# Kernel optimization log

Measured on AMD Instinct MI355X. Metric: run time of the kernel, lower is better.

Reference implementation:

```python
import jax, jax.numpy as jnp
import numpy as np

D_MODEL = 1024
N_HEADS = 16
HEAD_DIM = D_MODEL // N_HEADS  # 64


def _rotate_half(x):
    x1, x2 = jnp.split(x, 2, axis=-1)
    return jnp.concatenate((-x2, x1), axis=-1)


def setup_inputs() -> dict:
    key = jax.random.key(0)
    ks = jax.random.split(key, 9)
    B, S = 2, 2048
    sc = 1.0 / np.sqrt(D_MODEL)
    return {
        "x": jax.random.normal(ks[0], (B, S, D_MODEL), dtype=jnp.float32),
        "Wq": jax.random.normal(ks[1], (D_MODEL, D_MODEL), dtype=jnp.float32) * sc,
        "bq": jax.random.normal(ks[2], (D_MODEL,), dtype=jnp.float32) * 0.02,
        "Wk": jax.random.normal(ks[3], (D_MODEL, D_MODEL), dtype=jnp.float32) * sc,
        "bk": jax.random.normal(ks[4], (D_MODEL,), dtype=jnp.float32) * 0.02,
        "Wv": jax.random.normal(ks[5], (D_MODEL, D_MODEL), dtype=jnp.float32) * sc,
        "bv": jax.random.normal(ks[6], (D_MODEL,), dtype=jnp.float32) * 0.02,
        "Wo": jax.random.normal(ks[7], (D_MODEL, D_MODEL), dtype=jnp.float32) * sc,
        "bo": jax.random.normal(ks[8], (D_MODEL,), dtype=jnp.float32) * 0.02,
    }


def reference(x, Wq, bq, Wk, bk, Wv, bv, Wo, bo):
    B, S, _ = x.shape
    H, D = N_HEADS, HEAD_DIM
    # QKV projections -> [B, H, S, D]
    q = (x @ Wq + bq).reshape(B, S, H, D).transpose(0, 2, 1, 3)
    k = (x @ Wk + bk).reshape(B, S, H, D).transpose(0, 2, 1, 3)
    v = (x @ Wv + bv).reshape(B, S, H, D).transpose(0, 2, 1, 3)
    # Rotary embedding on head_dim
    inv_freq = 1.0 / (10000.0 ** (jnp.arange(0, D, 2, dtype=jnp.float32) / D))
    t = jnp.arange(S, dtype=jnp.float32)
    freqs = jnp.outer(t, inv_freq)                      # [S, D/2]
    emb = jnp.concatenate((freqs, freqs), axis=-1)      # [S, D]
    # Faithful to torch: cos/sin end up rank-5 [1,1,1,S,D], promoting q/k to [1,B,H,S,D]
    cos = jnp.cos(emb)[None, None, None]
    sin = jnp.sin(emb)[None, None, None]
    qe = q * cos + _rotate_half(q) * sin                # [1,B,H,S,D]
    ke = k * cos + _rotate_half(k) * sin                # [1,B,H,S,D]
    scores = jnp.matmul(qe, jnp.swapaxes(ke, -1, -2)) / np.sqrt(D).astype(np.float32)  # [1,B,H,S,S]
    attn = jax.nn.softmax(scores, axis=-1)
    out = jnp.matmul(attn, v)                           # [1,B,H,S,D] (v broadcast)
    # Faithful replication of torch transpose(1,2).contiguous().view(B,S,d_model)
    out = out.transpose(0, 2, 1, 3, 4).reshape(B, S, H * D)
    return out @ Wo + bo
```

## Files before the change

### kernel.cpp

```cpp
#include <hip/hip_runtime.h>
#include <hip/hip_bf16.h>
#include <stdint.h>

typedef __bf16 bf16;
typedef __bf16 bf16x8 __attribute__((ext_vector_type(8)));
typedef __bf16 bf16x4 __attribute__((ext_vector_type(4)));
typedef float  f32x4  __attribute__((ext_vector_type(4)));
typedef int    i32x4  __attribute__((ext_vector_type(4)));

#define MFMA16(a, b, c) __builtin_amdgcn_mfma_f32_16x16x32_bf16((a), (b), (c), 0, 0, 0)

#define GLOAD16(gp, lp) __builtin_amdgcn_global_load_lds(                     \
    (__attribute__((address_space(1))) void*)(gp),                            \
    (__attribute__((address_space(3))) void*)(lp), 16, 0, 0)


__global__ __launch_bounds__(256) void k_prep(
    const float* __restrict__ x,
    const float* __restrict__ Wq, const float* __restrict__ Wk,
    const float* __restrict__ Wv, const float* __restrict__ Wo,
    bf16* __restrict__ xb, bf16* __restrict__ wqkvt, bf16* __restrict__ wot,
    float* __restrict__ ct, float* __restrict__ st) {
    __shared__ float t[32][33];
    const int bid = blockIdx.x, tid = threadIdx.x;
    if (bid < 4096) {
        const int i = bid * 256 + tid;
        float4 v = ((const float4*)x)[i];
        bf16x4 o;
        o[0] = (bf16)v.x; o[1] = (bf16)v.y; o[2] = (bf16)v.z; o[3] = (bf16)v.w;
        ((bf16x4*)xb)[i] = o;
    } else if (bid < 4352) {
        const int i = (bid - 4096) * 256 + tid;
        const int s = i >> 5, j = i & 31;
        const float inv = expf(-(float)j * (9.210340371976184f / 32.0f));
        const float a = (float)s * inv;
        ct[i] = cosf(a);
        st[i] = sinf(a);
    } else {
        const int wb = bid - 4352;
        const int z = wb >> 10, tb = wb & 1023;
        const float* src = (z == 0) ? Wq : (z == 1) ? Wk : (z == 2) ? Wv : Wo;
        bf16* dst = (z < 3) ? wqkvt + (size_t)z * 1024 * 1024 : wot;
        const int bx = (tb & 31) * 32, by = (tb >> 5) * 32;
        const int tx = tid & 31, ty = tid >> 5;
#pragma unroll
        for (int i = 0; i < 32; i += 8)
            t[ty + i][tx] = src[(size_t)(by + ty + i) * 1024 + bx + tx];
        __syncthreads();
#pragma unroll
        for (int i = 0; i < 32; i += 8)
            dst[(size_t)(bx + ty + i) * 1024 + by + tx] = (bf16)t[tx][ty + i];
    }
}

__device__ __forceinline__ void gemm_loop(const bf16* __restrict__ A,
                                          const bf16* __restrict__ Bt,
                                          int m0, int n0,
                                          bf16* As, bf16* Bs,
                                          f32x4 (&acc)[4][4]) {
    const int tid  = threadIdx.x;
    const int w    = tid >> 6, lane = tid & 63;
    const int wr   = (w >> 1) * 64, wc = (w & 1) * 64;
    const int l15  = lane & 15, l4 = lane >> 4;
    const int srow = w * 16 + (lane >> 2);
    const int skol = 8 * ((lane & 3) ^ ((lane >> 3) & 3));
    const int rdb  = l15 * 32 + 8 * (l4 ^ ((l15 >> 1) & 3));
    const bf16* Ap = A  + (size_t)(m0 + srow) * 1024 + skol;
    const bf16* Bp = Bt + (size_t)(n0 + srow) * 1024 + skol;

#define GSTAGE(B, kt) do {                                                   \
        GLOAD16(Ap + (kt),         As + (B) * 4096 + w * 512);               \
        GLOAD16(Ap + 65536 + (kt), As + (B) * 4096 + 2048 + w * 512);        \
        GLOAD16(Bp + (kt),         Bs + (B) * 4096 + w * 512);               \
        GLOAD16(Bp + 65536 + (kt), Bs + (B) * 4096 + 2048 + w * 512);        \
    } while (0)

#define GTILE(t, B) do {                                                     \
        asm volatile("s_waitcnt vmcnt(0)" ::: "memory");                     \
        __builtin_amdgcn_s_barrier();                                        \
        if ((t) < 31) GSTAGE((B) ^ 1, ((t) + 1) * 32);                       \
        bf16x8 af[4], bfv[4];                                                \
        _Pragma("unroll")                                                    \
        for (int m = 0; m < 4; ++m)                                          \
            af[m] = *(const bf16x8*)(As + (B) * 4096 + (wr + 16 * m) * 32 + rdb); \
        _Pragma("unroll")                                                    \
        for (int n = 0; n < 4; ++n)                                          \
            bfv[n] = *(const bf16x8*)(Bs + (B) * 4096 + (wc + 16 * n) * 32 + rdb); \
        __builtin_amdgcn_s_setprio(1);                                       \
        _Pragma("unroll")                                                    \
        for (int m = 0; m < 4; ++m)                                          \
            _Pragma("unroll")                                                \
            for (int n = 0; n < 4; ++n)                                      \
                acc[m][n] = MFMA16(af[m], bfv[n], acc[m][n]);                \
        __builtin_amdgcn_s_setprio(0);                                       \
    } while (0)

    GSTAGE(0, 0);
    for (int t = 0; t < 32; t += 2) {
        GTILE(t, 0);
        GTILE(t + 1, 1);
    }
#undef GTILE
#undef GSTAGE
}

__global__ __launch_bounds__(256) void k_gemm_qkv(
    const bf16* __restrict__ X, const bf16* __restrict__ Wt,
    const float* __restrict__ bq, const float* __restrict__ bk,
    const float* __restrict__ bv,
    const float* __restrict__ ct, const float* __restrict__ st,
    bf16* __restrict__ qbuf, bf16* __restrict__ kbuf, bf16* __restrict__ vtb) {
    __shared__ __align__(16) bf16 As[2 * 4096];
    __shared__ __align__(16) bf16 Bs[2 * 4096];
    f32x4 acc[4][4] = {};
    const int nwg = gridDim.x * gridDim.y;
    const int wg  = blockIdx.y * gridDim.x + blockIdx.x;
    const int sw  = (wg & 7) * (nwg >> 3) + (wg >> 3);
    const int m0 = (sw / gridDim.x) * 128, n0 = (sw % gridDim.x) * 128;
    gemm_loop(X, Wt, m0, n0, As, Bs, acc);

    const int tid = threadIdx.x;
    const int w = tid >> 6, lane = tid & 63;
    const int wr = (w >> 1) * 64, wc = (w & 1) * 64;
    const int l15 = lane & 15, l4 = lane >> 4;

    const int featbase = n0 + wc;
    const int kind = featbase >> 10;
    const int col0 = featbase & 1023;
    const int h = col0 >> 6;
    const float* bias = (kind == 0) ? bq : (kind == 1) ? bk : bv;
    const float oscale = (kind == 0) ? 0.18033688011112042f : 1.0f;

#pragma unroll
    for (int m = 0; m < 4; ++m) {
#pragma unroll
        for (int j = 0; j < 4; ++j) {
            const int tok = m0 + wr + 16 * m + 4 * l4 + j;
            const int b = tok >> 11, s = tok & 2047;
            float vals[4];
#pragma unroll
            for (int n = 0; n < 4; ++n)
                vals[n] = acc[m][n][j] + bias[col0 + 16 * n + l15];
            if (kind < 2) {
                bf16* dst = (kind == 0) ? qbuf : kbuf;
                const size_t base = ((size_t)((b * 16 + h) * 2048 + s)) * 64;
#pragma unroll
                for (int n = 0; n < 4; ++n) {
                    const int dd = 16 * n + l15;
                    const int jr = dd & 31;
                    const float c = ct[s * 32 + jr], sn = st[s * 32 + jr];
                    const float other = vals[n ^ 2];
                    const float rot = (dd < 32) ? -other : other;
                    dst[base + dd] = (bf16)((vals[n] * c + rot * sn) * oscale);
                }
            } else {
                const int sp = (s & ~63) | ((s & 0x1C) << 1) | ((s & 0x20) >> 3) | (s & 3);
#pragma unroll
                for (int n = 0; n < 4; ++n) {
                    const int dd = 16 * n + l15;
                    vtb[((size_t)((b * 16 + h) * 64 + dd)) * 2048 + sp] = (bf16)vals[n];
                }
            }
        }
    }
}

__global__ __launch_bounds__(512) void k_attn(const bf16* __restrict__ qbuf,
                                              const bf16* __restrict__ kbuf,
                                              const bf16* __restrict__ vtb,
                                              bf16* __restrict__ ob) {
    __shared__ __align__(16) bf16 smem[2 * 2 * 2 * 4096];

    const int tid = threadIdx.x, w = tid >> 6, lane = tid & 63;
    const int team = w >> 2, wt = w & 3;
    const int l15 = lane & 15, l4 = lane >> 4;

    const int sid = blockIdx.x;
    const int bh  = (sid & 7) * 4 + ((sid >> 3) >> 4);
    const int qb0 = ((sid >> 3) & 15) * 128;
    const int b = bh >> 4, h = bh & 15;

    const bf16* qp = qbuf + ((size_t)bh * 2048 + qb0 + wt * 32 + l15) * 64 + 8 * l4;
    i32x4 qr00 = *(const i32x4*)qp;
    i32x4 qr01 = *(const i32x4*)(qp + 32);
    i32x4 qr10 = *(const i32x4*)(qp + 16 * 64);
    i32x4 qr11 = *(const i32x4*)(qp + 16 * 64 + 32);
    asm volatile("" :: "v"(qr00), "v"(qr01), "v"(qr10), "v"(qr11));
    asm volatile("s_waitcnt vmcnt(0)" ::: "memory");
    bf16x8 aq[2][2];
    aq[0][0] = __builtin_bit_cast(bf16x8, qr00);
    aq[0][1] = __builtin_bit_cast(bf16x8, qr01);
    aq[1][0] = __builtin_bit_cast(bf16x8, qr10);
    aq[1][1] = __builtin_bit_cast(bf16x8, qr11);

    bf16x8 ones;
#pragma unroll
    for (int i = 0; i < 8; ++i) ones[i] = (bf16)1.0f;

    f32x4 ao[2][4] = {};
    f32x4 lacc[2] = {};
    const f32x4 zf = {0.f, 0.f, 0.f, 0.f};

    const int r8   = lane >> 3;
    const int skol = 8 * ((lane & 7) ^ r8);
    const int rdb  = l15 * 64 + 32 * ((l15 >> 2) & 1) + 8 * (l4 ^ (l15 & 3));
    const bf16* kp = kbuf + (size_t)bh * 131072 + (size_t)team * 65536
                   + (size_t)(wt * 8 + r8) * 64 + skol;
    const bf16* vp = vtb  + (size_t)bh * 131072 + (size_t)(wt * 8 + r8) * 2048
                   + team * 1024 + skol;
    bf16* sK = smem + team * 16384;
    bf16* sV = smem + team * 16384 + 8192;
    const bf16* pK0 = sK + rdb;
    const bf16* pK1 = sK + (rdb ^ 32);
    const bf16* pV0 = sV + rdb;
    const bf16* pV1 = sV + (rdb ^ 32);

#define STAGE(B, t) do {                                                  \
        GLOAD16(kp + (size_t)(t) * 4096,        sK + (B) * 4096 + wt * 512);        \
        GLOAD16(kp + (size_t)(t) * 4096 + 2048, sK + (B) * 4096 + 2048 + wt * 512); \
        GLOAD16(vp + (t) * 64,                  sV + (B) * 4096 + wt * 512);        \
        GLOAD16(vp + 65536 + (t) * 64,          sV + (B) * 4096 + 2048 + wt * 512); \
    } while (0)

#define TILE(t, B) do {                                                       \
        asm volatile("s_waitcnt vmcnt(0)" ::: "memory");                      \
        __builtin_amdgcn_s_barrier();                                         \
        if ((t) < 15) STAGE((B) ^ 1, (t) + 1);                                \
        bf16x8 kfr[2][4], vfr[2][4];                                          \
        _Pragma("unroll")                                                     \
        for (int n = 0; n < 4; ++n) {                                         \
            kfr[0][n] = *(const bf16x8*)(pK0 + (B) * 4096 + n * 1024);        \
            kfr[1][n] = *(const bf16x8*)(pK1 + (B) * 4096 + n * 1024);        \
            vfr[0][n] = *(const bf16x8*)(pV0 + (B) * 4096 + n * 1024);        \
            vfr[1][n] = *(const bf16x8*)(pV1 + (B) * 4096 + n * 1024);        \
        }                                                                     \
        f32x4 sc[2][4];                                                       \
        __builtin_amdgcn_s_setprio(1);                                        \
        _Pragma("unroll")                                                     \
        for (int n = 0; n < 4; ++n) {                                         \
            sc[0][n] = MFMA16(kfr[0][n], aq[0][0], zf);                       \
            sc[1][n] = MFMA16(kfr[0][n], aq[1][0], zf);                       \
        }                                                                     \
        _Pragma("unroll")                                                     \
        for (int n = 0; n < 4; ++n) {                                         \
            sc[0][n] = MFMA16(kfr[1][n], aq[0][1], sc[0][n]);                 \
            sc[1][n] = MFMA16(kfr[1][n], aq[1][1], sc[1][n]);                 \
        }                                                                     \
        __builtin_amdgcn_s_setprio(0);                                        \
                  \
        bf16x8 ap[2][2];                                                      \
        _Pragma("unroll")                                                     \
        for (int f = 0; f < 2; ++f) {                                         \
            float e0[4], e1[4], e2[4], e3[4];                                 \
            _Pragma("unroll")                                                 \
            for (int r = 0; r < 4; ++r) {                                     \
                asm("v_exp_f32 %0, %1" : "=v"(e0[r]) : "v"(sc[f][0][r]));     \
                asm("v_exp_f32 %0, %1" : "=v"(e1[r]) : "v"(sc[f][1][r]));     \
                asm("v_exp_f32 %0, %1" : "=v"(e2[r]) : "v"(sc[f][2][r]));     \
                asm("v_exp_f32 %0, %1" : "=v"(e3[r]) : "v"(sc[f][3][r]));     \
            }                                                                 \
            unsigned q0, q1, q2, q3, q4, q5, q6, q7;                          \
            asm("v_cvt_pk_bf16_f32 %0, %1, %2" : "=v"(q0) : "v"(e0[0]), "v"(e0[1])); \
            asm("v_cvt_pk_bf16_f32 %0, %1, %2" : "=v"(q1) : "v"(e0[2]), "v"(e0[3])); \
            asm("v_cvt_pk_bf16_f32 %0, %1, %2" : "=v"(q2) : "v"(e2[0]), "v"(e2[1])); \
            asm("v_cvt_pk_bf16_f32 %0, %1, %2" : "=v"(q3) : "v"(e2[2]), "v"(e2[3])); \
            asm("v_cvt_pk_bf16_f32 %0, %1, %2" : "=v"(q4) : "v"(e1[0]), "v"(e1[1])); \
            asm("v_cvt_pk_bf16_f32 %0, %1, %2" : "=v"(q5) : "v"(e1[2]), "v"(e1[3])); \
            asm("v_cvt_pk_bf16_f32 %0, %1, %2" : "=v"(q6) : "v"(e3[0]), "v"(e3[1])); \
            asm("v_cvt_pk_bf16_f32 %0, %1, %2" : "=v"(q7) : "v"(e3[2]), "v"(e3[3])); \
            i32x4 w0 = {(int)q0, (int)q1, (int)q2, (int)q3};                  \
            i32x4 w1 = {(int)q4, (int)q5, (int)q6, (int)q7};                  \
            ap[f][0] = __builtin_bit_cast(bf16x8, w0);                        \
            ap[f][1] = __builtin_bit_cast(bf16x8, w1);                        \
        }                                                                     \
        __builtin_amdgcn_s_setprio(1);                                        \
        lacc[0] = MFMA16(ap[0][0], ones, lacc[0]);                            \
        lacc[0] = MFMA16(ap[0][1], ones, lacc[0]);                            \
        lacc[1] = MFMA16(ap[1][0], ones, lacc[1]);                            \
        lacc[1] = MFMA16(ap[1][1], ones, lacc[1]);                            \
        _Pragma("unroll")                                                     \
        for (int kk = 0; kk < 2; ++kk)                                        \
            _Pragma("unroll")                                                 \
            for (int n = 0; n < 4; ++n) {                                     \
                ao[0][n] = MFMA16(ap[0][kk], vfr[kk][n], ao[0][n]);           \
                ao[1][n] = MFMA16(ap[1][kk], vfr[kk][n], ao[1][n]);           \
            }                                                                 \
        __builtin_amdgcn_s_setprio(0);                                        \
    } while (0)

    STAGE(0, 0);
    for (int t = 0; t < 16; t += 2) {
        TILE(t, 0);
        TILE(t + 1, 1);
    }
#undef TILE
#undef STAGE

    float* mO = (float*)(smem + 16384);
    float* mL = (float*)smem;
    __syncthreads();
    if (team == 1) {
#pragma unroll
        for (int f = 0; f < 2; ++f) {
#pragma unroll
            for (int j = 0; j < 4; ++j) {
                const int row = wt * 32 + f * 16 + 4 * l4 + j;
#pragma unroll
                for (int n = 0; n < 4; ++n)
                    mO[row * 64 + 16 * n + l15] = ao[f][n][j];
                if (l15 == 0) mL[row] = lacc[f][j];
            }
        }
    }
    __syncthreads();
    if (team == 0) {
#pragma unroll
        for (int f = 0; f < 2; ++f) {
#pragma unroll
            for (int j = 0; j < 4; ++j) {
                const int row = wt * 32 + f * 16 + 4 * l4 + j;
                const float inv = 1.0f / (lacc[f][j] + mL[row]);
                const int s = qb0 + row;
                const size_t base = ((size_t)(h * 256 + b * 128 + (s >> 4))) * 1024
                                  + (s & 15) * 64;
#pragma unroll
                for (int n = 0; n < 4; ++n)
                    ob[base + 16 * n + l15] =
                        (bf16)((ao[f][n][j] + mO[row * 64 + 16 * n + l15]) * inv);
            }
        }
    }
}

__global__ __launch_bounds__(256) void k_gemm_out(const bf16* __restrict__ O,
                                                  const bf16* __restrict__ Wt,
                                                  const float* __restrict__ bo,
                                                  float* __restrict__ out) {
    __shared__ __align__(16) bf16 As[2 * 4096];
    __shared__ __align__(16) bf16 Bs[2 * 4096];
    f32x4 acc[4][4] = {};
    const int nwg = gridDim.x * gridDim.y;
    const int wg  = blockIdx.y * gridDim.x + blockIdx.x;
    const int sw  = (wg & 7) * (nwg >> 3) + (wg >> 3);
    const int m0 = (sw / gridDim.x) * 128, n0 = (sw % gridDim.x) * 128;
    gemm_loop(O, Wt, m0, n0, As, Bs, acc);

    const int tid = threadIdx.x;
    const int w = tid >> 6, lane = tid & 63;
    const int wr = (w >> 1) * 64, wc = (w & 1) * 64;
    const int l15 = lane & 15, l4 = lane >> 4;
#pragma unroll
    for (int m = 0; m < 4; ++m) {
#pragma unroll
        for (int j = 0; j < 4; ++j) {
            const int tok = m0 + wr + 16 * m + 4 * l4 + j;
#pragma unroll
            for (int n = 0; n < 4; ++n) {
                const int feat = n0 + wc + 16 * n + l15;
                out[(size_t)tok * 1024 + feat] = acc[m][n][j] + bo[feat];
            }
        }
    }
}

extern "C" void kernel_launch(void* const* d_in, const int* in_sizes, int n_in,
                              void* d_out, int out_size, void* d_ws, size_t ws_size,
                              hipStream_t stream) {
    (void)in_sizes; (void)n_in; (void)out_size; (void)ws_size;
    const float* x  = (const float*)d_in[0];
    const float* Wq = (const float*)d_in[1];
    const float* bq = (const float*)d_in[2];
    const float* Wk = (const float*)d_in[3];
    const float* bk = (const float*)d_in[4];
    const float* Wv = (const float*)d_in[5];
    const float* bv = (const float*)d_in[6];
    const float* Wo = (const float*)d_in[7];
    const float* bo = (const float*)d_in[8];
    float* out = (float*)d_out;

    char* p = (char*)d_ws;
    bf16* xb    = (bf16*)p;  p += (size_t)4096 * 1024 * 2;
    bf16* wqkvt = (bf16*)p;  p += (size_t)3072 * 1024 * 2;
    bf16* wot   = (bf16*)p;  p += (size_t)1024 * 1024 * 2;
    bf16* qbuf  = (bf16*)p;  p += (size_t)32 * 2048 * 64 * 2;
    bf16* kbuf  = (bf16*)p;  p += (size_t)32 * 2048 * 64 * 2;
    bf16* vtb   = (bf16*)p;  p += (size_t)32 * 64 * 2048 * 2;
    float* ct   = (float*)p; p += (size_t)2048 * 32 * 4;
    float* st   = (float*)p; p += (size_t)2048 * 32 * 4;
    bf16* obuf  = xb;

    k_prep<<<dim3(8448), dim3(256), 0, stream>>>(x, Wq, Wk, Wv, Wo,
                                                 xb, wqkvt, wot, ct, st);
    k_gemm_qkv<<<dim3(24, 32), dim3(256), 0, stream>>>(xb, wqkvt, bq, bk, bv,
                                                       ct, st, qbuf, kbuf, vtb);
    k_attn<<<dim3(512), dim3(512), 0, stream>>>(qbuf, kbuf, vtb, obuf);
    k_gemm_out<<<dim3(8, 32), dim3(256), 0, stream>>>(obuf, wot, bo, out);
}
```

Before: 121.2 us.

## Triple-buffer GEMM LDS staging with partial vmcnt waits

Replaces the double-buffered K loop in the shared GEMM routine with a three-stage LDS ring. Two tiles are kept in flight and each step waits only for the oldest one (vmcnt(4)), so global-to-LDS loads overlap MFMA work over a longer window. LDS use per block rises from 32KB to 48KB, which may lower occupancy. The loop is unrolled by three with an explicit two-tile epilogue.

```diff
diff --git a/kernel.cpp b/kernel.cpp
--- a/kernel.cpp
+++ b/kernel.cpp
@@ -75,10 +75,7 @@
         GLOAD16(Bp + 65536 + (kt), Bs + (B) * 4096 + 2048 + w * 512);        \
     } while (0)
 
-#define GTILE(t, B) do {                                                     \
-        asm volatile("s_waitcnt vmcnt(0)" ::: "memory");                     \
-        __builtin_amdgcn_s_barrier();                                        \
-        if ((t) < 31) GSTAGE((B) ^ 1, ((t) + 1) * 32);                       \
+#define GCOMP(B) do {                                                        \
         bf16x8 af[4], bfv[4];                                                \
         _Pragma("unroll")                                                    \
         for (int m = 0; m < 4; ++m)                                          \
@@ -96,11 +93,28 @@
     } while (0)
 
     GSTAGE(0, 0);
-    for (int t = 0; t < 32; t += 2) {
-        GTILE(t, 0);
-        GTILE(t + 1, 1);
-    }
-#undef GTILE
+    GSTAGE(1, 32);
+    for (int i = 0; i < 30; i += 3) {
+        asm volatile("s_waitcnt vmcnt(4)" ::: "memory");
+        __builtin_amdgcn_s_barrier();
+        GSTAGE(2, (i + 2) * 32);
+        GCOMP(0);
+        asm volatile("s_waitcnt vmcnt(4)" ::: "memory");
+        __builtin_amdgcn_s_barrier();
+        GSTAGE(0, (i + 3) * 32);
+        GCOMP(1);
+        asm volatile("s_waitcnt vmcnt(4)" ::: "memory");
+        __builtin_amdgcn_s_barrier();
+        GSTAGE(1, (i + 4) * 32);
+        GCOMP(2);
+    }
+    asm volatile("s_waitcnt vmcnt(4)" ::: "memory");
+    __builtin_amdgcn_s_barrier();
+    GCOMP(0);
+    asm volatile("s_waitcnt vmcnt(0)" ::: "memory");
+    __builtin_amdgcn_s_barrier();
+    GCOMP(1);
+#undef GCOMP
 #undef GSTAGE
 }
 
@@ -110,8 +124,8 @@
     const float* __restrict__ bv,
     const float* __restrict__ ct, const float* __restrict__ st,
     bf16* __restrict__ qbuf, bf16* __restrict__ kbuf, bf16* __restrict__ vtb) {
-    __shared__ __align__(16) bf16 As[2 * 4096];
-    __shared__ __align__(16) bf16 Bs[2 * 4096];
+    __shared__ __align__(16) bf16 As[3 * 4096];
+    __shared__ __align__(16) bf16 Bs[3 * 4096];
     f32x4 acc[4][4] = {};
     const int nwg = gridDim.x * gridDim.y;
     const int wg  = blockIdx.y * gridDim.x + blockIdx.x;
@@ -336,8 +350,8 @@
                                                   const bf16* __restrict__ Wt,
                                                   const float* __restrict__ bo,
                                                   float* __restrict__ out) {
-    __shared__ __align__(16) bf16 As[2 * 4096];
-    __shared__ __align__(16) bf16 Bs[2 * 4096];
+    __shared__ __align__(16) bf16 As[3 * 4096];
+    __shared__ __align__(16) bf16 Bs[3 * 4096];
     f32x4 acc[4][4] = {};
     const int nwg = gridDim.x * gridDim.y;
     const int wg  = blockIdx.y * gridDim.x + blockIdx.x;
```

Result: no change. 119.1 us (-1.7%).

## Use 128x64 tiles with three-stage LDS pipeline in output projection GEMM

Applied to the files above, without the earlier changes.

Replaces the shared gemm_loop in the output projection with an inline triple-buffered global-to-LDS pipeline and halves the N tile to 64, doubling the grid to 512 workgroups. The intent is better CU occupancy and latency hiding with prefetch depth two and raised wave priority around the MFMA bursts. Smaller tiles reduce per-workgroup data reuse and increase redundant loads of the activation rows.

```diff
diff --git a/kernel.cpp b/kernel.cpp
--- a/kernel.cpp
+++ b/kernel.cpp
@@ -336,26 +336,80 @@
                                                   const bf16* __restrict__ Wt,
                                                   const float* __restrict__ bo,
                                                   float* __restrict__ out) {
-    __shared__ __align__(16) bf16 As[2 * 4096];
-    __shared__ __align__(16) bf16 Bs[2 * 4096];
-    f32x4 acc[4][4] = {};
+    __shared__ __align__(16) bf16 As[3 * 4096];
+    __shared__ __align__(16) bf16 Bs[3 * 2048];
+    f32x4 acc[4][2] = {};
+
     const int nwg = gridDim.x * gridDim.y;
     const int wg  = blockIdx.y * gridDim.x + blockIdx.x;
     const int sw  = (wg & 7) * (nwg >> 3) + (wg >> 3);
-    const int m0 = (sw / gridDim.x) * 128, n0 = (sw % gridDim.x) * 128;
-    gemm_loop(O, Wt, m0, n0, As, Bs, acc);
-
-    const int tid = threadIdx.x;
-    const int w = tid >> 6, lane = tid & 63;
-    const int wr = (w >> 1) * 64, wc = (w & 1) * 64;
-    const int l15 = lane & 15, l4 = lane >> 4;
+    const int m0 = (sw / gridDim.x) * 128, n0 = (sw % gridDim.x) * 64;
+
+    const int tid  = threadIdx.x;
+    const int w    = tid >> 6, lane = tid & 63;
+    const int wr   = (w >> 1) * 64, wc = (w & 1) * 32;
+    const int l15  = lane & 15, l4 = lane >> 4;
+    const int srow = w * 16 + (lane >> 2);
+    const int skol = 8 * ((lane & 3) ^ ((lane >> 3) & 3));
+    const int rdb  = l15 * 32 + 8 * (l4 ^ ((l15 >> 1) & 3));
+    const bf16* Ap = O  + (size_t)(m0 + srow) * 1024 + skol;
+    const bf16* Bp = Wt + (size_t)(n0 + srow) * 1024 + skol;
+
+#define OSTAGE(B, kt) do {                                                   \
+        GLOAD16(Ap + (kt),         As + (B) * 4096 + w * 512);               \
+        GLOAD16(Ap + 65536 + (kt), As + (B) * 4096 + 2048 + w * 512);        \
+        GLOAD16(Bp + (kt),         Bs + (B) * 2048 + w * 512);               \
+    } while (0)
+
+#define OCOMP(B) do {                                                        \
+        bf16x8 af[4], bfv[2];                                                \
+        _Pragma("unroll")                                                    \
+        for (int m = 0; m < 4; ++m)                                          \
+            af[m] = *(const bf16x8*)(As + (B) * 4096 + (wr + 16 * m) * 32 + rdb); \
+        _Pragma("unroll")                                                    \
+        for (int n = 0; n < 2; ++n)                                          \
+            bfv[n] = *(const bf16x8*)(Bs + (B) * 2048 + (wc + 16 * n) * 32 + rdb); \
+        __builtin_amdgcn_s_setprio(1);                                       \
+        _Pragma("unroll")                                                    \
+        for (int m = 0; m < 4; ++m)                                          \
+            _Pragma("unroll")                                                \
+            for (int n = 0; n < 2; ++n)                                      \
+                acc[m][n] = MFMA16(af[m], bfv[n], acc[m][n]);                \
+        __builtin_amdgcn_s_setprio(0);                                       \
+    } while (0)
+
+    OSTAGE(0, 0);
+    OSTAGE(1, 32);
+    for (int i = 0; i < 30; i += 3) {
+        asm volatile("s_waitcnt vmcnt(3)" ::: "memory");
+        __builtin_amdgcn_s_barrier();
+        OSTAGE(2, (i + 2) * 32);
+        OCOMP(0);
+        asm volatile("s_waitcnt vmcnt(3)" ::: "memory");
+        __builtin_amdgcn_s_barrier();
+        OSTAGE(0, (i + 3) * 32);
+        OCOMP(1);
+        asm volatile("s_waitcnt vmcnt(3)" ::: "memory");
+        __builtin_amdgcn_s_barrier();
+        OSTAGE(1, (i + 4) * 32);
+        OCOMP(2);
+    }
+    asm volatile("s_waitcnt vmcnt(3)" ::: "memory");
+    __builtin_amdgcn_s_barrier();
+    OCOMP(0);
+    asm volatile("s_waitcnt vmcnt(0)" ::: "memory");
+    __builtin_amdgcn_s_barrier();
+    OCOMP(1);
+#undef OCOMP
+#undef OSTAGE
+
 #pragma unroll
     for (int m = 0; m < 4; ++m) {
 #pragma unroll
         for (int j = 0; j < 4; ++j) {
             const int tok = m0 + wr + 16 * m + 4 * l4 + j;
 #pragma unroll
-            for (int n = 0; n < 4; ++n) {
+            for (int n = 0; n < 2; ++n) {
                 const int feat = n0 + wc + 16 * n + l15;
                 out[(size_t)tok * 1024 + feat] = acc[m][n][j] + bo[feat];
             }
@@ -394,5 +448,5 @@
     k_gemm_qkv<<<dim3(24, 32), dim3(256), 0, stream>>>(xb, wqkvt, bq, bk, bv,
                                                        ct, st, qbuf, kbuf, vtb);
     k_attn<<<dim3(512), dim3(512), 0, stream>>>(qbuf, kbuf, vtb, obuf);
-    k_gemm_out<<<dim3(8, 32), dim3(256), 0, stream>>>(obuf, wot, bo, out);
-}
+    k_gemm_out<<<dim3(16, 32), dim3(256), 0, stream>>>(obuf, wot, bo, out);
+}
```

After: 118.4 us (median of 3 runs). 1.02x faster.
